# Kernel optimization log

Measured on AMD Instinct MI355X. Metric: run time of the kernel, lower is better.

Reference implementation:

```python
import jax, jax.numpy as jnp
import numpy as np

EPS_BN = 1e-5
EPS_LN = 1e-5

def _bn(x, gamma, beta, ch_axis):
    # training-mode BatchNorm: batch stats over all axes except ch_axis (biased var)
    axes = tuple(i for i in range(x.ndim) if i != ch_axis)
    mean = x.mean(axes, keepdims=True)
    var = x.var(axes, keepdims=True)
    shp = [1] * x.ndim; shp[ch_axis] = -1
    return (x - mean) / jnp.sqrt(var + EPS_BN) * gamma.reshape(shp) + beta.reshape(shp)

def _ln(x, gamma, beta):
    mean = x.mean(-1, keepdims=True)
    var = x.var(-1, keepdims=True)
    return (x - mean) / jnp.sqrt(var + EPS_LN) * gamma + beta

def _spline(x, knots, cps):
    # x: (B,S); knots, cps: (K,). Single-pass bucketize + gather + lerp,
    # equivalent to the torch per-interval masked loop (boundary points take
    # the right interval's t=0 value, identical result).
    K = knots.shape[0]
    xn = (x - jnp.min(x)) / (jnp.max(x) - jnp.min(x) + 1e-6)
    idx = jnp.clip(jnp.searchsorted(knots, xn, side='right') - 1, 0, K - 2)
    k0, k1 = knots[idx], knots[idx + 1]
    t = (xn - k0) / (k1 - k0)
    val = (1.0 - t) * cps[idx] + t * cps[idx + 1]
    in_range = (xn >= knots[0]) & (xn <= knots[-1])
    return jnp.where(in_range, val, 0.0)

def _mha(x, in_w, in_b, out_w, out_b, H):
    # torch nn.MultiheadAttention with batch_first=False: dim0 is the sequence.
    L, N, D = x.shape
    hd = D // H
    qkv = x @ in_w.T + in_b                       # (L,N,3D)
    q, k, v = jnp.split(qkv, 3, axis=-1)
    q = q.reshape(L, N, H, hd) * (1.0 / np.sqrt(hd))
    k = k.reshape(L, N, H, hd)
    v = v.reshape(L, N, H, hd)
    scores = jnp.einsum('lnhd,mnhd->nhlm', q, k)  # (N,H,L,L)
    attn = jax.nn.softmax(scores, axis=-1)
    out = jnp.einsum('nhlm,mnhd->lnhd', attn, v).reshape(L, N, D)
    return out @ out_w.T + out_b

def setup_inputs() -> dict:
    B, S, D, F, K, H = 32, 1024, 512, 8, 32, 8
    key = jax.random.key(0)
    ks = jax.random.split(key, 12)
    s = 0.02
    inp = {
        'x': jax.random.normal(ks[0], (B, S, D), jnp.float32),
        'in_w': jax.random.normal(ks[1], (3 * D, D), jnp.float32) * s,
        'in_b': jnp.zeros((3 * D,), jnp.float32),
        'out_w': jax.random.normal(ks[2], (D, D), jnp.float32) * s,
        'out_b': jnp.zeros((D,), jnp.float32),
        'attn_g': jnp.ones((D,), jnp.float32),
        'attn_beta': jnp.zeros((D,), jnp.float32),
        'proj_w': jax.random.normal(ks[3], (F, D), jnp.float32) * s,
        'proj_b': jnp.zeros((F,), jnp.float32),
        'pn_g': jnp.ones((F,), jnp.float32),
        'pn_beta': jnp.zeros((F,), jnp.float32),
        'knots': jnp.tile(jnp.linspace(0.0, 1.0, K, dtype=jnp.float32)[None, :], (F, 1)),
        'cps': jax.random.normal(ks[4], (F, K), jnp.float32) / np.sqrt(K),
        'gate_w': jax.random.normal(ks[5], (2 * D, F), jnp.float32) * s,
        'gate_b': jnp.zeros((2 * D,), jnp.float32),
        'gbn_g': jnp.ones((S,), jnp.float32),   # BatchNorm1d(2*d_model) hits dim1 = seq (= 2*d_model)
        'gbn_beta': jnp.zeros((S,), jnp.float32),
        'ln_g': jnp.ones((D,), jnp.float32),
        'ln_beta': jnp.zeros((D,), jnp.float32),
        'outp_w': jax.random.normal(ks[6], (D, D), jnp.float32) * s,
        'outp_b': jnp.zeros((D,), jnp.float32),
        'on_g': jnp.ones((D,), jnp.float32),
        'on_beta': jnp.zeros((D,), jnp.float32),
    }
    return inp

def reference(x, in_w, in_b, out_w, out_b, attn_g, attn_beta, proj_w, proj_b,
              pn_g, pn_beta, knots, cps, gate_w, gate_b, gbn_g, gbn_beta,
              ln_g, ln_beta, outp_w, outp_b, on_g, on_beta):
    H = 8
    attn_out = _mha(x, in_w, in_b, out_w, out_b, H)          # (B,S,D)
    attn_out = _bn(attn_out, attn_g, attn_beta, 2)
    projected = x @ proj_w.T + proj_b                         # (B,S,F)
    projected = _bn(projected, pn_g, pn_beta, 2)
    transformed = jax.vmap(_spline, in_axes=(2, 0, 0), out_axes=2)(projected, knots, cps)  # (B,S,F)
    h = transformed @ gate_w.T + gate_b                       # (B,S,2D)
    h = _bn(h, gbn_g, gbn_beta, 1)                            # channel axis = seq (torch quirk)
    a, b = jnp.split(h, 2, axis=-1)
    glu = a * jax.nn.sigmoid(b)                               # (B,S,D)
    gated = _ln(glu, ln_g, ln_beta)
    out = gated @ outp_w.T + outp_b
    out = _bn(out, on_g, on_beta, 2)
    return x + attn_out + out
```

## Files before the change

kernel.cpp:

```cpp
#include <hip/hip_runtime.h>
#include <math.h>


#define SOFF_AMEAN 0
#define SOFF_ARSTD 512
#define SOFF_OMEAN 1024
#define SOFF_ORSTD 1536
#define SOFF_PMEAN 2048
#define SOFF_PRSTD 2056
#define SOFF_FMIN  2064
#define SOFF_FMAX  2072
#define SOFF_SMEAN 2080
#define SOFF_SRSTD 3104
#define SOFF_G1    4128
#define SOFF_GB    4136
#define SOFF_SGB   4144
#define SOFF_QGB   4145
#define SOFF_G2    4160
#define SOFF_PART  4224

typedef short bf16x8_t __attribute__((ext_vector_type(8)));
typedef float f32x4_t __attribute__((ext_vector_type(4)));
typedef unsigned short us8_t __attribute__((ext_vector_type(8)));

__device__ __forceinline__ unsigned short f2bf(float f) {
  unsigned u = __float_as_uint(f);
  u = (u + 0x7FFFu + ((u >> 16) & 1u)) >> 16;
  return (unsigned short)u;
}
__device__ __forceinline__ float b2f(unsigned short u) {
  return __uint_as_float(((unsigned)u) << 16);
}

__global__ __launch_bounds__(256) void zero_kernel(float* __restrict__ p) {
  p[blockIdx.x * 256 + threadIdx.x] = 0.f;
}

__global__ __launch_bounds__(256) void cvt8_kernel(const float* __restrict__ src,
                                                   unsigned short* __restrict__ dst) {
  int i = blockIdx.x * 256 + threadIdx.x;
  float4 a = ((const float4*)src)[i * 2];
  float4 b = ((const float4*)src)[i * 2 + 1];
  us8_t o;
  o[0] = f2bf(a.x); o[1] = f2bf(a.y); o[2] = f2bf(a.z); o[3] = f2bf(a.w);
  o[4] = f2bf(b.x); o[5] = f2bf(b.y); o[6] = f2bf(b.z); o[7] = f2bf(b.w);
  *(us8_t*)(dst + (size_t)i * 8) = o;
}

template<int NT, bool OUT_BF16, bool STATS>
__global__ __launch_bounds__(256) void gemm_mfma_kernel(
    const unsigned short* __restrict__ A, const unsigned short* __restrict__ B,
    const float* __restrict__ bias, unsigned short* __restrict__ Cb,
    float* __restrict__ Cf, float* __restrict__ gstats, int N) {
  __shared__ unsigned short As[128 * 32];
  __shared__ unsigned short Bs[128 * 32];
  __shared__ float colred[256];
  const int bi = blockIdx.x;
  const int xcd = bi & 7, j = bi >> 3;
  const int m0 = (xcd * 32 + j / NT) * 128;
  const int n0 = (j % NT) * 128;
  const int t = threadIdx.x;
  const int w = t >> 6, lane = t & 63;
  const int wm = w >> 1, wn = w & 1;
  if (STATS) colred[t] = 0.f;
  f32x4_t acc[4][4];
#pragma unroll
  for (int i = 0; i < 4; ++i)
#pragma unroll
    for (int jj = 0; jj < 4; ++jj) acc[i][jj] = (f32x4_t){0.f, 0.f, 0.f, 0.f};

  const int lrow = lane >> 2;
  const int lk = (lane & 3) * 8;
  const unsigned short* ga = A + (size_t)(m0 + w * 32 + lrow) * 512 + lk;
  const unsigned short* gb = B + (size_t)(n0 + w * 32 + lrow) * 512 + lk;
  unsigned short* lA = &As[(w * 32) * 32];
  unsigned short* lB = &Bs[(w * 32) * 32];
  const int fr = lane & 15, fq = (lane >> 4) * 8;

  for (int k0 = 0; k0 < 512; k0 += 32) {
    __syncthreads();
    __builtin_amdgcn_global_load_lds(
        (const __attribute__((address_space(1))) void*)(ga + k0),
        (__attribute__((address_space(3))) void*)lA, 16, 0, 0);
    __builtin_amdgcn_global_load_lds(
        (const __attribute__((address_space(1))) void*)(ga + k0 + 16 * 512),
        (__attribute__((address_space(3))) void*)(lA + 16 * 32), 16, 0, 0);
    __builtin_amdgcn_global_load_lds(
        (const __attribute__((address_space(1))) void*)(gb + k0),
        (__attribute__((address_space(3))) void*)lB, 16, 0, 0);
    __builtin_amdgcn_global_load_lds(
        (const __attribute__((address_space(1))) void*)(gb + k0 + 16 * 512),
        (__attribute__((address_space(3))) void*)(lB + 16 * 32), 16, 0, 0);
    __syncthreads();
    bf16x8_t af[4], bf[4];
#pragma unroll
    for (int mi = 0; mi < 4; ++mi)
      af[mi] = *(const bf16x8_t*)&As[(wm * 64 + mi * 16 + fr) * 32 + fq];
#pragma unroll
    for (int ni = 0; ni < 4; ++ni)
      bf[ni] = *(const bf16x8_t*)&Bs[(wn * 64 + ni * 16 + fr) * 32 + fq];
#pragma unroll
    for (int mi = 0; mi < 4; ++mi)
#pragma unroll
      for (int ni = 0; ni < 4; ++ni)
        acc[mi][ni] = __builtin_amdgcn_mfma_f32_16x16x32_bf16(af[mi], bf[ni], acc[mi][ni], 0, 0, 0);
  }
  const int cr = (lane >> 4) * 4, cc = lane & 15;
#pragma unroll
  for (int ni = 0; ni < 4; ++ni) {
    int col = n0 + wn * 64 + ni * 16 + cc;
    float bv = bias[col];
    float lsum = 0.f, lsq = 0.f;
#pragma unroll
    for (int mi = 0; mi < 4; ++mi) {
#pragma unroll
      for (int jj = 0; jj < 4; ++jj) {
        int row = m0 + wm * 64 + mi * 16 + cr + jj;
        float v = acc[mi][ni][jj] + bv;
        if (OUT_BF16) Cb[(size_t)row * N + col] = f2bf(v);
        else          Cf[(size_t)row * N + col] = v;
        if (STATS) { lsum += v; lsq += v * v; }
      }
    }
    if (STATS) {
      lsum += __shfl_xor(lsum, 16); lsum += __shfl_xor(lsum, 32);
      lsq  += __shfl_xor(lsq, 16);  lsq  += __shfl_xor(lsq, 32);
      if (lane < 16) {
        int cidx = wn * 64 + ni * 16 + lane;
        atomicAdd(&colred[cidx], lsum);
        atomicAdd(&colred[128 + cidx], lsq);
      }
    }
  }
  if (STATS) {
    __syncthreads();
    if (t < 128) {
      atomicAdd(&gstats[n0 + t], colred[t]);
      atomicAdd(&gstats[512 + n0 + t], colred[128 + t]);
    }
  }
}

__global__ __launch_bounds__(512) void statsfin_kernel(const float* __restrict__ part,
                                                       float* __restrict__ stats, int off) {
  int t = threadIdx.x;
  float mean = part[t] / 32768.f;
  float var = part[512 + t] / 32768.f - mean * mean;
  stats[off + t] = mean;
  stats[off + 512 + t] = rsqrtf(var + 1e-5f);
}

__global__ __launch_bounds__(256) void attn2_kernel(const unsigned short* __restrict__ qkv,
                                                    unsigned short* __restrict__ ctxb) {
  const int n = blockIdx.x, h = blockIdx.y, t = threadIdx.x;
  __shared__ float qs[32 * 68], ks[32 * 68], vs[32 * 68], ss[32 * 33];
  const int l = t >> 3, j0 = (t & 7) * 8;
  size_t rowb = ((size_t)(l * 1024 + n)) * 1536 + h * 64 + j0;
  us8_t qv = *(const us8_t*)(qkv + rowb);
  us8_t kv = *(const us8_t*)(qkv + rowb + 512);
  us8_t vv = *(const us8_t*)(qkv + rowb + 1024);
#pragma unroll
  for (int j = 0; j < 8; ++j) {
    qs[l * 68 + j0 + j] = b2f(qv[j]) * 0.125f;
    ks[l * 68 + j0 + j] = b2f(kv[j]);
    vs[l * 68 + j0 + j] = b2f(vv[j]);
  }
  __syncthreads();
  for (int o = t; o < 1024; o += 256) {
    int ll = o >> 5, m = o & 31;
    const float4* q4 = (const float4*)&qs[ll * 68];
    const float4* k4 = (const float4*)&ks[m * 68];
    float s = 0.f;
#pragma unroll
    for (int dd = 0; dd < 16; ++dd) {
      float4 a = q4[dd], b = k4[dd];
      s += a.x * b.x + a.y * b.y + a.z * b.z + a.w * b.w;
    }
    ss[ll * 33 + m] = s;
  }
  __syncthreads();
  if (t < 32) {
    float mx = -3e38f;
    for (int m = 0; m < 32; ++m) mx = fmaxf(mx, ss[t * 33 + m]);
    float sum = 0.f;
    for (int m = 0; m < 32; ++m) { float e = __expf(ss[t * 33 + m] - mx); ss[t * 33 + m] = e; sum += e; }
    float inv = 1.f / sum;
    for (int m = 0; m < 32; ++m) ss[t * 33 + m] *= inv;
  }
  __syncthreads();
  float o[8] = {0.f, 0.f, 0.f, 0.f, 0.f, 0.f, 0.f, 0.f};
#pragma unroll 8
  for (int m = 0; m < 32; ++m) {
    float pm = ss[l * 33 + m];
    const float* vr = &vs[m * 68 + j0];
#pragma unroll
    for (int j = 0; j < 8; ++j) o[j] += pm * vr[j];
  }
  us8_t ov;
#pragma unroll
  for (int j = 0; j < 8; ++j) ov[j] = f2bf(o[j]);
  *(us8_t*)(ctxb + ((size_t)(l * 1024 + n)) * 512 + h * 64 + j0) = ov;
}

__global__ __launch_bounds__(256) void proj_kernel(const float* __restrict__ x,
    const float* __restrict__ pw, const float* __restrict__ pb, float* __restrict__ p) {
  int blk = blockIdx.x, t = threadIdx.x;
  int r0 = blk * 64;
  __shared__ float xsp[64 * 33];
  __shared__ float pwc[8 * 33];
  int l = t >> 2, fg = t & 3;
  float acc0 = 0.f, acc1 = 0.f;
  for (int k0 = 0; k0 < 512; k0 += 32) {
    __syncthreads();
    for (int i = t; i < 2048; i += 256) { int ll = i >> 5, kk = i & 31; xsp[ll * 33 + kk] = x[(size_t)(r0 + ll) * 512 + k0 + kk]; }
    { int ff = t >> 5, kk = t & 31; pwc[ff * 33 + kk] = pw[ff * 512 + k0 + kk]; }
    __syncthreads();
#pragma unroll 8
    for (int kk = 0; kk < 32; ++kk) {
      float xv = xsp[l * 33 + kk];
      acc0 += xv * pwc[(fg * 2) * 33 + kk];
      acc1 += xv * pwc[(fg * 2 + 1) * 33 + kk];
    }
  }
  float2 o; o.x = acc0 + pb[fg * 2]; o.y = acc1 + pb[fg * 2 + 1];
  *(float2*)&p[(r0 + l) * 8 + fg * 2] = o;
}

__global__ __launch_bounds__(256) void projstats_kernel(const float* __restrict__ p,
                                                        float* __restrict__ part) {
  int t = threadIdx.x, blk = blockIdx.x;
  int f = t & 7;
  float s = 0.f, s2 = 0.f;
  for (int r = blk * 32 + (t >> 3); r < 32768; r += 2048) { float v = p[r * 8 + f]; s += v; s2 += v * v; }
  __shared__ float red[256], red2[256];
  red[t] = s; red2[t] = s2; __syncthreads();
  for (int off = 128; off >= 8; off >>= 1) { if (t < off) { red[t] += red[t + off]; red2[t] += red2[t + off]; } __syncthreads(); }
  if (t < 8) { part[blk * 16 + t] = red[t]; part[blk * 16 + 8 + t] = red2[t]; }
}
__global__ void projfin_kernel(const float* __restrict__ part, float* __restrict__ stats) {
  int t = threadIdx.x;
  if (t < 8) {
    float s = 0.f, s2 = 0.f;
    for (int b = 0; b < 64; ++b) { s += part[b * 16 + t]; s2 += part[b * 16 + 8 + t]; }
    float mean = s / 32768.f;
    float var = s2 / 32768.f - mean * mean;
    stats[SOFF_PMEAN + t] = mean;
    stats[SOFF_PRSTD + t] = rsqrtf(var + 1e-5f);
  }
}

__global__ __launch_bounds__(256) void bnminmax_kernel(float* __restrict__ p,
    const float* __restrict__ stats, const float* __restrict__ png,
    const float* __restrict__ pnb, float* __restrict__ part) {
  int t = threadIdx.x, blk = blockIdx.x;
  int i0 = blk * 256 + t;
  int f = i0 & 7;
  float k1 = stats[SOFF_PRSTD + f] * png[f];
  float k0 = pnb[f] - stats[SOFF_PMEAN + f] * k1;
  float mn = 3e38f, mx = -3e38f;
  for (int i = i0; i < 262144; i += 16384) {
    float v = p[i] * k1 + k0;
    p[i] = v;
    mn = fminf(mn, v); mx = fmaxf(mx, v);
  }
  __shared__ float rmn[256], rmx[256];
  rmn[t] = mn; rmx[t] = mx; __syncthreads();
  for (int off = 128; off >= 8; off >>= 1) {
    if (t < off) { rmn[t] = fminf(rmn[t], rmn[t + off]); rmx[t] = fmaxf(rmx[t], rmx[t + off]); }
    __syncthreads();
  }
  if (t < 8) { part[blk * 16 + t] = rmn[t]; part[blk * 16 + 8 + t] = rmx[t]; }
}
__global__ void minmaxfin_kernel(const float* __restrict__ part, float* __restrict__ stats) {
  int t = threadIdx.x;
  if (t < 8) {
    float mn = 3e38f, mx = -3e38f;
    for (int b = 0; b < 64; ++b) { mn = fminf(mn, part[b * 16 + t]); mx = fmaxf(mx, part[b * 16 + 8 + t]); }
    stats[SOFF_FMIN + t] = mn;
    stats[SOFF_FMAX + t] = mx;
  }
}

__global__ __launch_bounds__(256) void spline_kernel(float* __restrict__ p,
    const float* __restrict__ knots, const float* __restrict__ cps,
    const float* __restrict__ stats) {
  __shared__ float ksh[8 * 33], csh[8 * 33];
  int t = threadIdx.x;
  { int f = t >> 5, j = t & 31; ksh[f * 33 + j] = knots[t]; csh[f * 33 + j] = cps[t]; }
  __syncthreads();
  int i = blockIdx.x * 256 + t;
  int f = i & 7;
  float xv = p[i];
  float mn = stats[SOFF_FMIN + f], mx = stats[SOFF_FMAX + f];
  float xn = (xv - mn) / (mx - mn + 1e-6f);
  const float* kn = &ksh[f * 33];
  const float* cp = &csh[f * 33];
  int pcnt = 0;
#pragma unroll
  for (int j = 0; j < 32; ++j) pcnt += (kn[j] <= xn) ? 1 : 0;
  int idx = pcnt - 1;
  idx = idx < 0 ? 0 : (idx > 30 ? 30 : idx);
  float k0v = kn[idx], k1v = kn[idx + 1];
  float tt = (xn - k0v) / (k1v - k0v);
  float val = (1.f - tt) * cp[idx] + tt * cp[idx + 1];
  bool inr = (xn >= kn[0]) && (xn <= kn[31]);
  p[i] = inr ? val : 0.f;
}

__global__ __launch_bounds__(256) void gateprep_kernel(const float* __restrict__ gw,
    const float* __restrict__ gb, float* __restrict__ stats) {
  int b = blockIdx.x, t = threadIdx.x;
  __shared__ float red[256];
  float s = 0.f;
  if (b < 64) {
    int f1 = b >> 3, f2 = b & 7;
    for (int j = t; j < 1024; j += 256) s += gw[j * 8 + f1] * gw[j * 8 + f2];
  } else if (b < 72) {
    int f = b - 64;
    for (int j = t; j < 1024; j += 256) s += gw[j * 8 + f];
  } else if (b < 80) {
    int f = b - 72;
    for (int j = t; j < 1024; j += 256) s += gb[j] * gw[j * 8 + f];
  } else if (b == 80) {
    for (int j = t; j < 1024; j += 256) s += gb[j];
  } else {
    for (int j = t; j < 1024; j += 256) s += gb[j] * gb[j];
  }
  red[t] = s; __syncthreads();
  for (int off = 128; off > 0; off >>= 1) { if (t < off) red[t] += red[t + off]; __syncthreads(); }
  if (t == 0) {
    float v = red[0];
    if (b < 64) stats[SOFF_G2 + b] = v;
    else if (b < 72) stats[SOFF_G1 + (b - 64)] = v;
    else if (b < 80) stats[SOFF_GB + (b - 72)] = v;
    else if (b == 80) stats[SOFF_SGB] = v;
    else stats[SOFF_QGB] = v;
  }
}

__global__ __launch_bounds__(256) void sstats_kernel(const float* __restrict__ tbuf,
                                                     float* __restrict__ stats) {
  int s = blockIdx.x, t = threadIdx.x;
  __shared__ float tv[256];
  __shared__ float red[256];
  __shared__ float T1[8];
  __shared__ float Ms[64];
  int b = t >> 3, f = t & 7;
  tv[t] = tbuf[(b * 1024 + s) * 8 + f];
  __syncthreads();
  red[t] = tv[t]; __syncthreads();
  for (int off = 128; off >= 8; off >>= 1) { if (t < off) red[t] += red[t + off]; __syncthreads(); }
  if (t < 8) T1[t] = red[t];
  if (t < 64) {
    int f1 = t >> 3, f2 = t & 7; float sM = 0.f;
    for (int bb = 0; bb < 32; ++bb) sM += tv[bb * 8 + f1] * tv[bb * 8 + f2];
    Ms[t] = sM;
  }
  __syncthreads();
  if (t == 0) {
    float sh = 0.f, s2 = 0.f;
    for (int ff = 0; ff < 8; ++ff) {
      sh += stats[SOFF_G1 + ff] * T1[ff];
      s2 += 2.f * stats[SOFF_GB + ff] * T1[ff];
    }
    sh += 32.f * stats[SOFF_SGB];
    for (int i = 0; i < 64; ++i) s2 += Ms[i] * stats[SOFF_G2 + i];
    s2 += 32.f * stats[SOFF_QGB];
    float mean = sh / 32768.f;
    float var = s2 / 32768.f - mean * mean;
    stats[SOFF_SMEAN + s] = mean;
    stats[SOFF_SRSTD + s] = rsqrtf(var + 1e-5f);
  }
}

__global__ __launch_bounds__(256) void gluln_kernel(const float* __restrict__ tbuf,
    const float* __restrict__ gw, const float* __restrict__ gb,
    const float* __restrict__ stats, const float* __restrict__ gbng,
    const float* __restrict__ gbnb, const float* __restrict__ lng,
    const float* __restrict__ lnb, unsigned short* __restrict__ gatedb) {
  const int t = threadIdx.x, wave = t >> 6, lane = t & 63;
  for (int rr = 0; rr < 4; ++rr) {
    const int r = blockIdx.x * 16 + wave * 4 + rr;
    const int s = r & 1023;
    float4 tA = *(const float4*)&tbuf[r * 8];
    float4 tB = *(const float4*)&tbuf[r * 8 + 4];
    float smean = stats[SOFF_SMEAN + s], srstd = stats[SOFF_SRSTD + s];
    float k1 = srstd * gbng[s];
    float k0 = gbnb[s] - smean * k1;
    float g[8];
    float sum = 0.f, sq = 0.f;
#pragma unroll
    for (int i = 0; i < 8; ++i) {
      int c = i * 64 + lane;
      float4 wa0 = *(const float4*)&gw[c * 8];
      float4 wa1 = *(const float4*)&gw[c * 8 + 4];
      float4 wb0 = *(const float4*)&gw[(c + 512) * 8];
      float4 wb1 = *(const float4*)&gw[(c + 512) * 8 + 4];
      float ha = tA.x * wa0.x + tA.y * wa0.y + tA.z * wa0.z + tA.w * wa0.w
               + tB.x * wa1.x + tB.y * wa1.y + tB.z * wa1.z + tB.w * wa1.w + gb[c];
      float hb = tA.x * wb0.x + tA.y * wb0.y + tA.z * wb0.z + tA.w * wb0.w
               + tB.x * wb1.x + tB.y * wb1.y + tB.z * wb1.z + tB.w * wb1.w + gb[c + 512];
      ha = ha * k1 + k0;
      hb = hb * k1 + k0;
      float gv = ha / (1.f + __expf(-hb));
      g[i] = gv; sum += gv; sq += gv * gv;
    }
#pragma unroll
    for (int m = 32; m >= 1; m >>= 1) { sum += __shfl_xor(sum, m); sq += __shfl_xor(sq, m); }
    float mean = sum * (1.f / 512.f);
    float rstd = rsqrtf(sq * (1.f / 512.f) - mean * mean + 1e-5f);
#pragma unroll
    for (int i = 0; i < 8; ++i) {
      int c = i * 64 + lane;
      gatedb[(size_t)r * 512 + c] = f2bf((g[i] - mean) * rstd * lng[c] + lnb[c]);
    }
  }
}

__global__ __launch_bounds__(256) void final_kernel(const float* __restrict__ x,
    const float* __restrict__ attn, const float* __restrict__ outl,
    const float* __restrict__ stats, const float* __restrict__ ag,
    const float* __restrict__ ab, const float* __restrict__ og,
    const float* __restrict__ ob, float* __restrict__ y) {
  int idx = blockIdx.x * 256 + threadIdx.x;
  int c4 = (idx & 127) * 4;
  float4 xv = ((const float4*)x)[idx];
  float4 av = ((const float4*)attn)[idx];
  float4 ov = ((const float4*)outl)[idx];
  float4 am = *(const float4*)&stats[SOFF_AMEAN + c4];
  float4 ar = *(const float4*)&stats[SOFF_ARSTD + c4];
  float4 om = *(const float4*)&stats[SOFF_OMEAN + c4];
  float4 orr = *(const float4*)&stats[SOFF_ORSTD + c4];
  float4 g1 = *(const float4*)&ag[c4];
  float4 b1 = *(const float4*)&ab[c4];
  float4 g2 = *(const float4*)&og[c4];
  float4 b2 = *(const float4*)&ob[c4];
  float4 o;
  o.x = xv.x + (av.x - am.x) * ar.x * g1.x + b1.x + (ov.x - om.x) * orr.x * g2.x + b2.x;
  o.y = xv.y + (av.y - am.y) * ar.y * g1.y + b1.y + (ov.y - om.y) * orr.y * g2.y + b2.y;
  o.z = xv.z + (av.z - am.z) * ar.z * g1.z + b1.z + (ov.z - om.z) * orr.z * g2.z + b2.z;
  o.w = xv.w + (av.w - am.w) * ar.w * g1.w + b1.w + (ov.w - om.w) * orr.w * g2.w + b2.w;
  ((float4*)y)[idx] = o;
}

extern "C" void kernel_launch(void* const* d_in, const int* in_sizes, int n_in,
                              void* d_out, int out_size, void* d_ws, size_t ws_size,
                              hipStream_t stream) {
  (void)in_sizes; (void)n_in; (void)out_size; (void)ws_size;
  const float* x        = (const float*)d_in[0];
  const float* in_w     = (const float*)d_in[1];
  const float* in_b     = (const float*)d_in[2];
  const float* out_w    = (const float*)d_in[3];
  const float* out_b    = (const float*)d_in[4];
  const float* attn_g   = (const float*)d_in[5];
  const float* attn_bt  = (const float*)d_in[6];
  const float* proj_w   = (const float*)d_in[7];
  const float* proj_b   = (const float*)d_in[8];
  const float* pn_g     = (const float*)d_in[9];
  const float* pn_bt    = (const float*)d_in[10];
  const float* knots    = (const float*)d_in[11];
  const float* cps      = (const float*)d_in[12];
  const float* gate_w   = (const float*)d_in[13];
  const float* gate_b   = (const float*)d_in[14];
  const float* gbn_g    = (const float*)d_in[15];
  const float* gbn_bt   = (const float*)d_in[16];
  const float* ln_g     = (const float*)d_in[17];
  const float* ln_bt    = (const float*)d_in[18];
  const float* outp_w   = (const float*)d_in[19];
  const float* outp_b   = (const float*)d_in[20];
  const float* on_g     = (const float*)d_in[21];
  const float* on_bt    = (const float*)d_in[22];

  float* out = (float*)d_out;
  unsigned short* xb      = (unsigned short*)d_ws;
  unsigned short* qkv_b   = xb + 16777216;
  unsigned short* ctx_b   = qkv_b + 50331648;
  unsigned short* wqkv_b  = ctx_b + 16777216;
  unsigned short* wout_b  = wqkv_b + 786432;
  unsigned short* woutp_b = wout_b + 262144;
  float* proj  = (float*)(woutp_b + 262144);
  float* stats = proj + 262144;
  float* part  = stats + SOFF_PART;
  float* partA  = part;
  float* partO  = part + 1024;
  float* partP  = part + 2048;
  float* partMM = part + 3072;
  float* attnf = (float*)qkv_b;
  unsigned short* gated_b = xb;

  zero_kernel<<<dim3(8), dim3(256), 0, stream>>>(part);
  cvt8_kernel<<<dim3(8192), dim3(256), 0, stream>>>(x, xb);
  cvt8_kernel<<<dim3(384), dim3(256), 0, stream>>>(in_w, wqkv_b);
  cvt8_kernel<<<dim3(128), dim3(256), 0, stream>>>(out_w, wout_b);
  cvt8_kernel<<<dim3(128), dim3(256), 0, stream>>>(outp_w, woutp_b);
  gemm_mfma_kernel<12, true, false><<<dim3(3072), dim3(256), 0, stream>>>(
      xb, wqkv_b, in_b, qkv_b, nullptr, nullptr, 1536);
  attn2_kernel<<<dim3(1024, 8), dim3(256), 0, stream>>>(qkv_b, ctx_b);
  gemm_mfma_kernel<4, false, true><<<dim3(1024), dim3(256), 0, stream>>>(
      ctx_b, wout_b, out_b, nullptr, attnf, partA, 512);
  statsfin_kernel<<<dim3(1), dim3(512), 0, stream>>>(partA, stats, SOFF_AMEAN);
  proj_kernel<<<dim3(512), dim3(256), 0, stream>>>(x, proj_w, proj_b, proj);
  projstats_kernel<<<dim3(64), dim3(256), 0, stream>>>(proj, partP);
  projfin_kernel<<<dim3(1), dim3(64), 0, stream>>>(partP, stats);
  bnminmax_kernel<<<dim3(64), dim3(256), 0, stream>>>(proj, stats, pn_g, pn_bt, partMM);
  minmaxfin_kernel<<<dim3(1), dim3(64), 0, stream>>>(partMM, stats);
  spline_kernel<<<dim3(1024), dim3(256), 0, stream>>>(proj, knots, cps, stats);
  gateprep_kernel<<<dim3(88), dim3(256), 0, stream>>>(gate_w, gate_b, stats);
  sstats_kernel<<<dim3(1024), dim3(256), 0, stream>>>(proj, stats);
  gluln_kernel<<<dim3(2048), dim3(256), 0, stream>>>(proj, gate_w, gate_b, stats,
                                                     gbn_g, gbn_bt, ln_g, ln_bt, gated_b);
  gemm_mfma_kernel<4, false, true><<<dim3(1024), dim3(256), 0, stream>>>(
      gated_b, woutp_b, outp_b, nullptr, out, partO, 512);
  statsfin_kernel<<<dim3(1), dim3(512), 0, stream>>>(partO, stats, SOFF_OMEAN);
  final_kernel<<<dim3(16384), dim3(256), 0, stream>>>(x, attnf, out, stats,
                                                      attn_g, attn_bt, on_g, on_bt, out);
}
```

Before: 521.4 us.

## Replace 128x128 GEMM with double-buffered 256x256 swizzled MFMA kernel

The bf16 MFMA GEMM moves from 128x128 tiles, 256 threads and a K-step of 32 to 256x256 tiles, 512 threads and a K-step of 64. Shared memory is now double-buffered, so the next K tile is loaded while MFMAs run on the current one. Loads use an XOR swizzle to avoid LDS bank conflicts, and wave priority is raised around MFMA groups. Column statistics now go straight to global atomics per wave instead of through a shared reduction. The aim is more data reuse per tile and better overlap of loads with compute, at the cost of 128KB of LDS per block, heavy register pressure and far fewer blocks in the grid (256 for the N=512 GEMMs).

Measured after the change: 534.0 us. 1.02x slower.

```diff
diff --git a/kernel.cpp b/kernel.cpp
--- a/kernel.cpp
+++ b/kernel.cpp
@@ -32,6 +32,8 @@
   return __uint_as_float(((unsigned)u) << 16);
 }
 
+#define BARR do { asm volatile("" ::: "memory"); __builtin_amdgcn_s_barrier(); asm volatile("" ::: "memory"); } while (0)
+
 __global__ __launch_bounds__(256) void zero_kernel(float* __restrict__ p) {
   p[blockIdx.x * 256 + threadIdx.x] = 0.f;
 }
@@ -48,63 +50,96 @@
 }
 
 template<int NT, bool OUT_BF16, bool STATS>
-__global__ __launch_bounds__(256) void gemm_mfma_kernel(
+__global__ __launch_bounds__(512, 2) void gemm256_kernel(
     const unsigned short* __restrict__ A, const unsigned short* __restrict__ B,
     const float* __restrict__ bias, unsigned short* __restrict__ Cb,
     float* __restrict__ Cf, float* __restrict__ gstats, int N) {
-  __shared__ unsigned short As[128 * 32];
-  __shared__ unsigned short Bs[128 * 32];
-  __shared__ float colred[256];
+  __shared__ unsigned short As[2][256 * 64];
+  __shared__ unsigned short Bs[2][256 * 64];
   const int bi = blockIdx.x;
-  const int xcd = bi & 7, j = bi >> 3;
-  const int m0 = (xcd * 32 + j / NT) * 128;
-  const int n0 = (j % NT) * 128;
+  const int xcd = bi & 7, jb = bi >> 3;
+  const int m0 = (xcd * 16 + jb / NT) * 256;
+  const int n0 = (jb % NT) * 256;
   const int t = threadIdx.x;
   const int w = t >> 6, lane = t & 63;
-  const int wm = w >> 1, wn = w & 1;
-  if (STATS) colred[t] = 0.f;
-  f32x4_t acc[4][4];
-#pragma unroll
-  for (int i = 0; i < 4; ++i)
+  const int wm = w >> 2, wn = w & 3;
+
+  const int srow = lane >> 3;
+  const int sgo = ((lane & 7) ^ srow) * 8;
+  const unsigned short* gA = A + (size_t)(m0 + w * 32 + srow) * 512 + sgo;
+  const unsigned short* gB = B + (size_t)(n0 + w * 32 + srow) * 512 + sgo;
+
+  const int fr = lane & 15, g = lane >> 4;
+  const int swz = fr & 7;
+
+  f32x4_t acc[8][4];
+#pragma unroll
+  for (int i = 0; i < 8; ++i)
 #pragma unroll
     for (int jj = 0; jj < 4; ++jj) acc[i][jj] = (f32x4_t){0.f, 0.f, 0.f, 0.f};
 
-  const int lrow = lane >> 2;
-  const int lk = (lane & 3) * 8;
-  const unsigned short* ga = A + (size_t)(m0 + w * 32 + lrow) * 512 + lk;
-  const unsigned short* gb = B + (size_t)(n0 + w * 32 + lrow) * 512 + lk;
-  unsigned short* lA = &As[(w * 32) * 32];
-  unsigned short* lB = &Bs[(w * 32) * 32];
-  const int fr = lane & 15, fq = (lane >> 4) * 8;
-
-  for (int k0 = 0; k0 < 512; k0 += 32) {
-    __syncthreads();
-    __builtin_amdgcn_global_load_lds(
-        (const __attribute__((address_space(1))) void*)(ga + k0),
-        (__attribute__((address_space(3))) void*)lA, 16, 0, 0);
-    __builtin_amdgcn_global_load_lds(
-        (const __attribute__((address_space(1))) void*)(ga + k0 + 16 * 512),
-        (__attribute__((address_space(3))) void*)(lA + 16 * 32), 16, 0, 0);
-    __builtin_amdgcn_global_load_lds(
-        (const __attribute__((address_space(1))) void*)(gb + k0),
-        (__attribute__((address_space(3))) void*)lB, 16, 0, 0);
-    __builtin_amdgcn_global_load_lds(
-        (const __attribute__((address_space(1))) void*)(gb + k0 + 16 * 512),
-        (__attribute__((address_space(3))) void*)(lB + 16 * 32), 16, 0, 0);
-    __syncthreads();
-    bf16x8_t af[4], bf[4];
-#pragma unroll
-    for (int mi = 0; mi < 4; ++mi)
-      af[mi] = *(const bf16x8_t*)&As[(wm * 64 + mi * 16 + fr) * 32 + fq];
+#define STAGE(SX, KO) do { \
+  _Pragma("unroll") for (int jj = 0; jj < 4; ++jj) { \
+    __builtin_amdgcn_global_load_lds( \
+        (const __attribute__((address_space(1))) void*)(gA + (size_t)jj * 8 * 512 + (KO)), \
+        (__attribute__((address_space(3))) void*)&As[SX][(w * 32 + jj * 8) * 64], 16, 0, 0); \
+    __builtin_amdgcn_global_load_lds( \
+        (const __attribute__((address_space(1))) void*)(gB + (size_t)jj * 8 * 512 + (KO)), \
+        (__attribute__((address_space(3))) void*)&Bs[SX][(w * 32 + jj * 8) * 64], 16, 0, 0); \
+  } \
+} while (0)
+
+#define RDA(MI0) do { \
+  _Pragma("unroll") for (int m2 = 0; m2 < 2; ++m2) \
+    _Pragma("unroll") for (int ks = 0; ks < 2; ++ks) \
+      af[m2][ks] = *(const bf16x8_t*)&as[((wm * 128 + (MI0 + m2) * 16 + fr) * 64) + (((ks * 4 + g) ^ swz) * 8)]; \
+} while (0)
+
+#define QUAD(MI0) do { \
+  __builtin_amdgcn_s_setprio(1); \
+  _Pragma("unroll") for (int ks = 0; ks < 2; ++ks) \
+    _Pragma("unroll") for (int m2 = 0; m2 < 2; ++m2) \
+      _Pragma("unroll") for (int ni = 0; ni < 4; ++ni) \
+        acc[MI0 + m2][ni] = __builtin_amdgcn_mfma_f32_16x16x32_bf16(af[m2][ks], bfr[ni][ks], acc[MI0 + m2][ni], 0, 0, 0); \
+  __builtin_amdgcn_s_setprio(0); \
+} while (0)
+
+  STAGE(0, (size_t)0);
+  asm volatile("s_waitcnt vmcnt(0)" ::: "memory");
+  BARR;
+
+#pragma unroll 2
+  for (int kt = 0; kt < 8; ++kt) {
+    const int sd = kt & 1;
+    const unsigned short* as = &As[sd][0];
+    const unsigned short* bs = &Bs[sd][0];
+    bf16x8_t bfr[4][2], af[2][2];
+
 #pragma unroll
     for (int ni = 0; ni < 4; ++ni)
-      bf[ni] = *(const bf16x8_t*)&Bs[(wn * 64 + ni * 16 + fr) * 32 + fq];
-#pragma unroll
-    for (int mi = 0; mi < 4; ++mi)
-#pragma unroll
-      for (int ni = 0; ni < 4; ++ni)
-        acc[mi][ni] = __builtin_amdgcn_mfma_f32_16x16x32_bf16(af[mi], bf[ni], acc[mi][ni], 0, 0, 0);
-  }
+#pragma unroll
+      for (int ks = 0; ks < 2; ++ks)
+        bfr[ni][ks] = *(const bf16x8_t*)&bs[((wn * 64 + ni * 16 + fr) * 64) + (((ks * 4 + g) ^ swz) * 8)];
+    RDA(0);
+    if (kt < 7) STAGE(sd ^ 1, (size_t)(kt + 1) * 64);
+    BARR;
+    QUAD(0);
+    BARR;
+    RDA(2);
+    BARR;
+    QUAD(2);
+    BARR;
+    RDA(4);
+    BARR;
+    QUAD(4);
+    BARR;
+    RDA(6);
+    BARR;
+    QUAD(6);
+    if (kt < 7) asm volatile("s_waitcnt vmcnt(0)" ::: "memory");
+    BARR;
+  }
+
   const int cr = (lane >> 4) * 4, cc = lane & 15;
 #pragma unroll
   for (int ni = 0; ni < 4; ++ni) {
@@ -112,10 +147,10 @@
     float bv = bias[col];
     float lsum = 0.f, lsq = 0.f;
 #pragma unroll
-    for (int mi = 0; mi < 4; ++mi) {
+    for (int mi = 0; mi < 8; ++mi) {
 #pragma unroll
       for (int jj = 0; jj < 4; ++jj) {
-        int row = m0 + wm * 64 + mi * 16 + cr + jj;
+        int row = m0 + wm * 128 + mi * 16 + cr + jj;
         float v = acc[mi][ni][jj] + bv;
         if (OUT_BF16) Cb[(size_t)row * N + col] = f2bf(v);
         else          Cf[(size_t)row * N + col] = v;
@@ -126,19 +161,14 @@
       lsum += __shfl_xor(lsum, 16); lsum += __shfl_xor(lsum, 32);
       lsq  += __shfl_xor(lsq, 16);  lsq  += __shfl_xor(lsq, 32);
       if (lane < 16) {
-        int cidx = wn * 64 + ni * 16 + lane;
-        atomicAdd(&colred[cidx], lsum);
-        atomicAdd(&colred[128 + cidx], lsq);
+        atomicAdd(&gstats[col], lsum);
+        atomicAdd(&gstats[512 + col], lsq);
       }
     }
   }
-  if (STATS) {
-    __syncthreads();
-    if (t < 128) {
-      atomicAdd(&gstats[n0 + t], colred[t]);
-      atomicAdd(&gstats[512 + n0 + t], colred[128 + t]);
-    }
-  }
+#undef STAGE
+#undef RDA
+#undef QUAD
 }
 
 __global__ __launch_bounds__(512) void statsfin_kernel(const float* __restrict__ part,
@@ -493,10 +523,10 @@
   cvt8_kernel<<<dim3(384), dim3(256), 0, stream>>>(in_w, wqkv_b);
   cvt8_kernel<<<dim3(128), dim3(256), 0, stream>>>(out_w, wout_b);
   cvt8_kernel<<<dim3(128), dim3(256), 0, stream>>>(outp_w, woutp_b);
-  gemm_mfma_kernel<12, true, false><<<dim3(3072), dim3(256), 0, stream>>>(
+  gemm256_kernel<6, true, false><<<dim3(768), dim3(512), 0, stream>>>(
       xb, wqkv_b, in_b, qkv_b, nullptr, nullptr, 1536);
   attn2_kernel<<<dim3(1024, 8), dim3(256), 0, stream>>>(qkv_b, ctx_b);
-  gemm_mfma_kernel<4, false, true><<<dim3(1024), dim3(256), 0, stream>>>(
+  gemm256_kernel<2, false, true><<<dim3(256), dim3(512), 0, stream>>>(
       ctx_b, wout_b, out_b, nullptr, attnf, partA, 512);
   statsfin_kernel<<<dim3(1), dim3(512), 0, stream>>>(partA, stats, SOFF_AMEAN);
   proj_kernel<<<dim3(512), dim3(256), 0, stream>>>(x, proj_w, proj_b, proj);
@@ -509,7 +539,7 @@
   sstats_kernel<<<dim3(1024), dim3(256), 0, stream>>>(proj, stats);
   gluln_kernel<<<dim3(2048), dim3(256), 0, stream>>>(proj, gate_w, gate_b, stats,
                                                      gbn_g, gbn_bt, ln_g, ln_bt, gated_b);
-  gemm_mfma_kernel<4, false, true><<<dim3(1024), dim3(256), 0, stream>>>(
+  gemm256_kernel<2, false, true><<<dim3(256), dim3(512), 0, stream>>>(
       gated_b, woutp_b, outp_b, nullptr, out, partO, 512);
   statsfin_kernel<<<dim3(1), dim3(512), 0, stream>>>(partO, stats, SOFF_OMEAN);
   final_kernel<<<dim3(16384), dim3(256), 0, stream>>>(x, attnf, out, stats,
```
